# Performance work log

Measured on AMD Instinct MI355X. Metric: run time of the kernel, lower is better.

Reference implementation:

```python
import jax, jax.numpy as jnp
import numpy as np

MAX_WAVELENGTH = 10000.0
NUM_HEADS = 15
NUM_KV_HEADS = 5
HEAD_DIM = 64


def apply_rope(x, positions):
    """RoPE: x [B, L, H, D], positions [B, L] (int)."""
    d_half = x.shape[-1] // 2
    x = x.astype(jnp.float32)
    freq_exponents = (2.0 / x.shape[-1]) * jnp.arange(d_half, dtype=jnp.float32)
    timescale = MAX_WAVELENGTH ** freq_exponents  # [d_half]
    radians = positions[..., None].astype(jnp.float32) / timescale  # [B, L, d_half]
    radians = radians[..., None, :]  # [B, L, 1, d_half]
    sin, cos = jnp.sin(radians), jnp.cos(radians)
    x1, x2 = x[..., :d_half], x[..., d_half:]
    return jnp.concatenate([x1 * cos - x2 * sin, x2 * cos + x1 * sin], axis=-1)


def setup_inputs() -> dict:
    key = jax.random.key(0)
    k1, k2, k3, k4 = jax.random.split(key, 4)
    B, L = 2, 2048
    query_states = jax.random.normal(k1, (B, L, NUM_HEADS, HEAD_DIM), dtype=jnp.float32)
    key_states = jax.random.normal(k2, (B, L, NUM_KV_HEADS, HEAD_DIM), dtype=jnp.float32)
    value_states = jax.random.normal(k3, (B, L, NUM_KV_HEADS, HEAD_DIM), dtype=jnp.float32)
    positions = jnp.sort(jax.random.randint(k4, (B, L), 0, L, dtype=jnp.int32), axis=-1)
    # Causal (prefix-LM) boolean mask [B, L, L]
    attention_mask = jnp.broadcast_to(jnp.tril(jnp.ones((L, L), dtype=bool)), (B, L, L))
    return {
        "query_states": query_states,
        "key_states": key_states,
        "value_states": value_states,
        "positions": positions,
        "attention_mask": attention_mask,
    }


def reference(query_states, key_states, value_states, positions, attention_mask):
    B, L = query_states.shape[0], query_states.shape[1]
    groups = NUM_HEADS // NUM_KV_HEADS  # 3

    # RoPE on Q and K (eager, per original module)
    q = apply_rope(query_states, positions)  # [B, L, 15, 64] fp32
    k = apply_rope(key_states, positions)    # [B, L, 5, 64]  fp32

    # GQA expansion: [B, L, Kv, D] -> [B, L, Kv*groups, D]
    k = jnp.repeat(k, groups, axis=2)
    v = jnp.repeat(value_states, groups, axis=2).astype(jnp.float32)

    # Scores in fp32: [B, H, Lq, Lk]
    scores = jnp.einsum("bqhd,bkhd->bhqk", q, k) * (HEAD_DIM ** -0.5)
    big_neg = jnp.finfo(jnp.float32).min
    scores = jnp.where(attention_mask[:, None, :, :], scores, big_neg)
    probs = jax.nn.softmax(scores, axis=-1)

    out = jnp.einsum("bhqk,bkhd->bqhd", probs, v)  # [B, L, H, D]
    return out.reshape(B, L, NUM_HEADS * HEAD_DIM)  # [B, L, 960]
```

## Files before the change

kernel.cpp:

```cpp
#include <hip/hip_runtime.h>
#include <math.h>

#define NB 2
#define NL 2048
#define NHQ 15
#define NKV 5
#define HD 64
#define NT 32
#define GRP 3
#define PST 72
#define NG 16
#define SLOTF 2080

typedef __attribute__((ext_vector_type(8))) short short8;
typedef __attribute__((ext_vector_type(4))) float floatx4;

#define ROPE_C 0.28782313662425575f
#define QSCALE 0.18033688011116016f

__device__ __forceinline__ ushort f2bf(float x) {
    unsigned u = __builtin_bit_cast(unsigned, x);
    u = (u + 0x7FFFu + ((u >> 16) & 1u)) >> 16;
    return (ushort)u;
}
__device__ __forceinline__ unsigned pk2(float a, float b) {
    unsigned ua = __builtin_bit_cast(unsigned, a) + 0x8000u;
    unsigned ub = __builtin_bit_cast(unsigned, b) + 0x8000u;
    return __builtin_amdgcn_perm(ub, ua, 0x07060302u);
}
__device__ __forceinline__ void async16(ushort* lds, const ushort* g) {
    __builtin_amdgcn_global_load_lds(
        (const __attribute__((address_space(1))) unsigned int*)g,
        (__attribute__((address_space(3))) unsigned int*)lds, 16, 0, 0);
}

union U8  { short8 v; ushort u[8]; };
union F8  { float4 f4[2]; float f[8]; };

__global__ __launch_bounds__(256)
void prep_kv(const float* __restrict__ K, const float* __restrict__ V,
             const int* __restrict__ pos, ushort* __restrict__ Kr,
             ushort* __restrict__ Vr) {
    __shared__ float Vs[64][65];
    const int bid = blockIdx.x, t = threadIdx.x;
    if (bid < NB * NKV * NT) {
        int b = bid / (NKV * NT), rem = bid % (NKV * NT);
        int h = rem / NT, k0 = (rem % NT) * 64;
        int j = t >> 2, c0 = t & 3;
        int row = k0 + j;
        const float* src = K + ((size_t)((b * NL + row) * NKV + h)) * HD;
        int db = c0 * 8;
        F8 x1, x2;
        x1.f4[0] = *(const float4*)&src[db];
        x1.f4[1] = *(const float4*)&src[db + 4];
        x2.f4[0] = *(const float4*)&src[db + 32];
        x2.f4[1] = *(const float4*)&src[db + 36];
        float ps = (float)pos[b * NL + row];
        U8 lo, hi;
#pragma unroll
        for (int i = 0; i < 8; ++i) {
            float inv = __expf((float)(db + i) * -ROPE_C);
            float sn, cs; __sincosf(ps * inv, &sn, &cs);
            lo.u[i] = f2bf(x1.f[i] * cs - x2.f[i] * sn);
            hi.u[i] = f2bf(x2.f[i] * cs + x1.f[i] * sn);
        }
        ushort* dst = Kr + (size_t)bid * 4096;
        *(short8*)&dst[(j * 8 + (c0 ^ (j & 7))) * 8]       = lo.v;
        *(short8*)&dst[(j * 8 + ((c0 + 4) ^ (j & 7))) * 8] = hi.v;
    } else {
        int vb = bid - NB * NKV * NT;
        int b = vb / (NKV * NT), rem = vb % (NKV * NT);
        int h = rem / NT, k0 = (rem % NT) * 64;
#pragma unroll
        for (int it = 0; it < 4; ++it) {
            int e = t + it * 256;
            int j = e >> 4, d4 = (e & 15) * 4;
            *(float4*)&Vs[j][d4] =
                *(const float4*)&V[((size_t)((b * NL + k0 + j) * NKV + h)) * HD + d4];
        }
        __syncthreads();
        ushort* dst = Vr + (size_t)vb * 4096;
#pragma unroll
        for (int it = 0; it < 2; ++it) {
            int o = t + it * 256;
            int d = o >> 3, c = o & 7, j0 = c * 8;
            U8 r;
#pragma unroll
            for (int k = 0; k < 8; ++k) r.u[k] = f2bf(Vs[j0 + k][d]);
            *(short8*)&dst[(d * 8 + (c ^ (d & 7))) * 8] = r.v;
        }
    }
}

__global__ __launch_bounds__(256, 4)
void attn_partial(const float* __restrict__ Q, const ushort* __restrict__ Kr,
                  const ushort* __restrict__ Vr, const int* __restrict__ pos,
                  float* __restrict__ Pw, int CH, int TOT) {
    __shared__ __align__(16) ushort Kb[4096];
    __shared__ __align__(16) ushort Vb[4096];
    __shared__ __align__(16) ushort Pb[4][2][16 * PST];

    const int t = threadIdx.x;
    const int w = t >> 6, lane = t & 63;
    const int l16 = lane & 15, quad = lane >> 4;
    const int h = blockIdx.y, b = blockIdx.z;
    const int kvh = h / GRP;
    const int fidx = TOT - 1 - (int)blockIdx.x;

    int g = 0, chunk = fidx;
    for (; g < NG; ++g) {
        int nc = (2 * g + 2 + CH - 1) / CH;
        if (chunk < nc) break;
        chunk -= nc;
    }
    const int ntg = 2 * g + 2;
    const int kb0 = chunk * CH;
    int kb1 = kb0 + CH; if (kb1 > ntg) kb1 = ntg;
    const int qi = 4 * g + w;
    const int ntw = (qi >> 1) + 1;
    const int r0 = qi * 32;

    short8 Qa[2][2];
#pragma unroll
    for (int rf = 0; rf < 2; ++rf) {
        int row = r0 + rf * 16 + l16;
        const float* src = Q + ((size_t)((b * NL + row) * NHQ + h)) * HD;
        int db = quad * 8;
        F8 x1, x2;
        x1.f4[0] = *(const float4*)&src[db];
        x1.f4[1] = *(const float4*)&src[db + 4];
        x2.f4[0] = *(const float4*)&src[db + 32];
        x2.f4[1] = *(const float4*)&src[db + 36];
        float ps = (float)pos[b * NL + row];
        union { short8 v; unsigned u[4]; } lo, hi;
#pragma unroll
        for (int i = 0; i < 8; i += 2) {
            float inv0 = __expf((float)(db + i) * -ROPE_C);
            float inv1 = __expf((float)(db + i + 1) * -ROPE_C);
            float sn0, cs0, sn1, cs1;
            __sincosf(ps * inv0, &sn0, &cs0);
            __sincosf(ps * inv1, &sn1, &cs1);
            float l0 = (x1.f[i] * cs0 - x2.f[i] * sn0) * QSCALE;
            float l1 = (x1.f[i + 1] * cs1 - x2.f[i + 1] * sn1) * QSCALE;
            float h0 = (x2.f[i] * cs0 + x1.f[i] * sn0) * QSCALE;
            float h1 = (x2.f[i + 1] * cs1 + x1.f[i + 1] * sn1) * QSCALE;
            lo.u[i >> 1] = pk2(l0, l1);
            hi.u[i >> 1] = pk2(h0, h1);
        }
        Qa[rf][0] = lo.v;
        Qa[rf][1] = hi.v;
    }

    floatx4 O[2][4];
    float lsum[2] = {0.f, 0.f};
#pragma unroll
    for (int rf = 0; rf < 2; ++rf)
#pragma unroll
        for (int d = 0; d < 4; ++d) O[rf][d] = (floatx4){0.f, 0.f, 0.f, 0.f};

    const ushort* Kt0 = Kr + (size_t)((b * NKV + kvh) * NT) * 4096;
    const ushort* Vt0 = Vr + (size_t)((b * NKV + kvh) * NT) * 4096;
    const int swz8[2] = { ((quad)     ^ (l16 & 7)) * 8,
                          ((quad + 4) ^ (l16 & 7)) * 8 };

    for (int kb = kb0; kb < kb1; ++kb) {
        {
            const ushort* Kt = Kt0 + (size_t)kb * 4096;
            const ushort* Vt = Vt0 + (size_t)kb * 4096;
            int so = w * 1024;
#pragma unroll
            for (int i2 = 0; i2 < 2; ++i2) {
                int uo = so + i2 * 512;
                async16(&Kb[uo], Kt + uo + lane * 8);
                async16(&Vb[uo], Vt + uo + lane * 8);
            }
        }
        __syncthreads();

        if (kb < ntw) {
            floatx4 S[2][4];
#pragma unroll
            for (int rf = 0; rf < 2; ++rf)
#pragma unroll
                for (int c = 0; c < 4; ++c) S[rf][c] = (floatx4){0.f, 0.f, 0.f, 0.f};
#pragma unroll
            for (int s = 0; s < 2; ++s)
#pragma unroll
                for (int c = 0; c < 4; ++c) {
                    short8 kfv = *(const short8*)&Kb[(c * 16 + l16) * 64 + swz8[s]];
                    S[0][c] = __builtin_amdgcn_mfma_f32_16x16x32_bf16(kfv, Qa[0][s], S[0][c], 0, 0, 0);
                    S[1][c] = __builtin_amdgcn_mfma_f32_16x16x32_bf16(kfv, Qa[1][s], S[1][c], 0, 0, 0);
                }

            const bool diag = (kb == ntw - 1);
#pragma unroll
            for (int rf = 0; rf < 2; ++rf) {
                int qrow = r0 + rf * 16 + l16;
                float acc = 0.f;
#pragma unroll
                for (int c = 0; c < 4; ++c) {
                    float p[4];
#pragma unroll
                    for (int r = 0; r < 4; ++r) {
                        int key = kb * 64 + c * 16 + quad * 4 + r;
                        float sv = S[rf][c][r];
                        if (diag && key > qrow) sv = -1e30f;
                        p[r] = exp2f(sv);
                        acc += p[r];
                    }
                    *(uint2*)&Pb[w][rf][l16 * PST + c * 16 + quad * 4] =
                        make_uint2(pk2(p[0], p[1]), pk2(p[2], p[3]));
                }
                lsum[rf] += acc;
            }

#pragma unroll
            for (int s = 0; s < 2; ++s) {
                short8 pf0 = *(const short8*)&Pb[w][0][l16 * PST + s * 32 + quad * 8];
                short8 pf1 = *(const short8*)&Pb[w][1][l16 * PST + s * 32 + quad * 8];
#pragma unroll
                for (int d = 0; d < 4; ++d) {
                    short8 vfv = *(const short8*)&Vb[(d * 16 + l16) * 64 + swz8[s]];
                    O[0][d] = __builtin_amdgcn_mfma_f32_16x16x32_bf16(vfv, pf0, O[0][d], 0, 0, 0);
                    O[1][d] = __builtin_amdgcn_mfma_f32_16x16x32_bf16(vfv, pf1, O[1][d], 0, 0, 0);
                }
            }
        }
        __syncthreads();
    }

    float* slot = Pw + (((size_t)(b * NHQ + h) * TOT + fidx) * 4 + w) * SLOTF;
#pragma unroll
    for (int rf = 0; rf < 2; ++rf) {
#pragma unroll
        for (int d = 0; d < 4; ++d) {
            float4 o = make_float4(O[rf][d][0], O[rf][d][1], O[rf][d][2], O[rf][d][3]);
            *(float4*)&slot[(rf * 16 + l16) * 64 + d * 16 + quad * 4] = o;
        }
        float ls = lsum[rf];
        ls += __shfl_xor(ls, 16, 64);
        ls += __shfl_xor(ls, 32, 64);
        if (quad == 0) slot[2048 + rf * 16 + l16] = ls;
    }
}

__global__ __launch_bounds__(256)
void combine(const float* __restrict__ Pw, float* __restrict__ out,
             int CH, int TOT) {
    __shared__ float ls[32];
    const int qi = blockIdx.x;
    const int bh = blockIdx.y;
    const int b = bh / NHQ, h = bh % NHQ;
    const int g = qi >> 2, w = qi & 3;
    const int nch = (2 * g + 2 + CH - 1) / CH;
    int pfx = 0;
    for (int gg = 0; gg < g; ++gg) pfx += (2 * gg + 2 + CH - 1) / CH;
    const float* base = Pw + (((size_t)bh * TOT + pfx) * 4 + w) * SLOTF;

    const int t = threadIdx.x;
    const int rl = t >> 3, d0 = (t & 7) * 8;
    float a[8];
#pragma unroll
    for (int k = 0; k < 8; ++k) a[k] = 0.f;
    float lacc = 0.f;
    for (int c = 0; c < nch; ++c) {
        const float* pb = base + (size_t)c * 4 * SLOTF;
        float4 x0 = *(const float4*)&pb[rl * 64 + d0];
        float4 x1 = *(const float4*)&pb[rl * 64 + d0 + 4];
        a[0] += x0.x; a[1] += x0.y; a[2] += x0.z; a[3] += x0.w;
        a[4] += x1.x; a[5] += x1.y; a[6] += x1.z; a[7] += x1.w;
        if (t < 32) lacc += pb[2048 + t];
    }
    if (t < 32) ls[t] = lacc;
    __syncthreads();
    float rinv = 1.0f / ls[rl];
    float* op = out + (size_t)(b * NL + qi * 32 + rl) * (NHQ * HD) + h * HD + d0;
    *(float4*)&op[0] = make_float4(a[0] * rinv, a[1] * rinv, a[2] * rinv, a[3] * rinv);
    *(float4*)&op[4] = make_float4(a[4] * rinv, a[5] * rinv, a[6] * rinv, a[7] * rinv);
}

extern "C" void kernel_launch(void* const* d_in, const int* in_sizes, int n_in,
                              void* d_out, int out_size, void* d_ws, size_t ws_size,
                              hipStream_t stream) {
    const float* Q   = (const float*)d_in[0];
    const float* K   = (const float*)d_in[1];
    const float* V   = (const float*)d_in[2];
    const int*   pos = (const int*)d_in[3];
    ushort* Kr = (ushort*)d_ws;
    ushort* Vr = Kr + (size_t)NB * NKV * NT * 4096;
    float*  Pw = (float*)(Vr + (size_t)NB * NKV * NT * 4096);
    float*  out = (float*)d_out;
    const size_t prepBytes = (size_t)2 * NB * NKV * NT * 4096 * sizeof(ushort);

    int CH = 32, TOT = NG;
    const int ladder[3] = {4, 8, 16};
    for (int i = 0; i < 3; ++i) {
        int ch = ladder[i], tot = 0;
        for (int gq = 0; gq < NG; ++gq) tot += (2 * gq + 2 + ch - 1) / ch;
        size_t need = prepBytes + (size_t)NB * NHQ * tot * 4 * SLOTF * sizeof(float);
        if (need <= ws_size) { CH = ch; TOT = tot; break; }
    }
    if (CH == 32) { TOT = NG; }

    prep_kv<<<2 * NB * NKV * NT, 256, 0, stream>>>(K, V, pos, Kr, Vr);
    dim3 grid(TOT, NHQ, NB);
    attn_partial<<<grid, 256, 0, stream>>>(Q, Kr, Vr, pos, Pw, CH, TOT);
    combine<<<dim3(NL / 32, NB * NHQ), 256, 0, stream>>>(Pw, out, CH, TOT);
}
```

Baseline: 160.6 us.

## Double-buffer K/V tiles and write single-chunk query groups directly to output

Adds ping-pong LDS buffers for K and V so the next tile's async load is issued before computing on the current one, hiding global load latency. Query groups whose key range fits in a single chunk now normalize and write the final output directly, and the combine kernel is launched only for the remaining groups. The split-size ladder drops the 4-tile option, giving fewer, larger chunks. This doubles K/V LDS use, which may lower occupancy, and coarser chunks reduce parallelism for long rows.

Measured after the change: 154.2 us. 1.04x faster.

```diff
diff --git a/kernel.cpp b/kernel.cpp
--- a/kernel.cpp
+++ b/kernel.cpp
@@ -95,9 +95,10 @@
 __global__ __launch_bounds__(256, 4)
 void attn_partial(const float* __restrict__ Q, const ushort* __restrict__ Kr,
                   const ushort* __restrict__ Vr, const int* __restrict__ pos,
-                  float* __restrict__ Pw, int CH, int TOT) {
-    __shared__ __align__(16) ushort Kb[4096];
-    __shared__ __align__(16) ushort Vb[4096];
+                  float* __restrict__ Pw, float* __restrict__ out,
+                  int CH, int TOT) {
+    __shared__ __align__(16) ushort Kb[2][4096];
+    __shared__ __align__(16) ushort Vb[2][4096];
     __shared__ __align__(16) ushort Pb[4][2][16 * PST];
 
     const int t = threadIdx.x;
@@ -114,6 +115,7 @@
         chunk -= nc;
     }
     const int ntg = 2 * g + 2;
+    const int nc  = (ntg + CH - 1) / CH;
     const int kb0 = chunk * CH;
     int kb1 = kb0 + CH; if (kb1 > ntg) kb1 = ntg;
     const int qi = 4 * g + w;
@@ -162,20 +164,28 @@
     const ushort* Vt0 = Vr + (size_t)((b * NKV + kvh) * NT) * 4096;
     const int swz8[2] = { ((quad)     ^ (l16 & 7)) * 8,
                           ((quad + 4) ^ (l16 & 7)) * 8 };
-
-    for (int kb = kb0; kb < kb1; ++kb) {
-        {
-            const ushort* Kt = Kt0 + (size_t)kb * 4096;
-            const ushort* Vt = Vt0 + (size_t)kb * 4096;
-            int so = w * 1024;
-#pragma unroll
-            for (int i2 = 0; i2 < 2; ++i2) {
-                int uo = so + i2 * 512;
-                async16(&Kb[uo], Kt + uo + lane * 8);
-                async16(&Vb[uo], Vt + uo + lane * 8);
-            }
-        }
-        __syncthreads();
+    const int so = w * 1024;
+
+    {
+        const ushort* Kt = Kt0 + (size_t)kb0 * 4096;
+        const ushort* Vt = Vt0 + (size_t)kb0 * 4096;
+        async16(&Kb[0][so],       Kt + so + lane * 8);
+        async16(&Kb[0][so + 512], Kt + so + 512 + lane * 8);
+        async16(&Vb[0][so],       Vt + so + lane * 8);
+        async16(&Vb[0][so + 512], Vt + so + 512 + lane * 8);
+    }
+    __syncthreads();
+
+    int p = 0;
+    for (int kb = kb0; kb < kb1; ++kb, p ^= 1) {
+        if (kb + 1 < kb1) {
+            const ushort* Kt = Kt0 + (size_t)(kb + 1) * 4096;
+            const ushort* Vt = Vt0 + (size_t)(kb + 1) * 4096;
+            async16(&Kb[p ^ 1][so],       Kt + so + lane * 8);
+            async16(&Kb[p ^ 1][so + 512], Kt + so + 512 + lane * 8);
+            async16(&Vb[p ^ 1][so],       Vt + so + lane * 8);
+            async16(&Vb[p ^ 1][so + 512], Vt + so + 512 + lane * 8);
+        }
 
         if (kb < ntw) {
             floatx4 S[2][4];
@@ -187,7 +197,7 @@
             for (int s = 0; s < 2; ++s)
 #pragma unroll
                 for (int c = 0; c < 4; ++c) {
-                    short8 kfv = *(const short8*)&Kb[(c * 16 + l16) * 64 + swz8[s]];
+                    short8 kfv = *(const short8*)&Kb[p][(c * 16 + l16) * 64 + swz8[s]];
                     S[0][c] = __builtin_amdgcn_mfma_f32_16x16x32_bf16(kfv, Qa[0][s], S[0][c], 0, 0, 0);
                     S[1][c] = __builtin_amdgcn_mfma_f32_16x16x32_bf16(kfv, Qa[1][s], S[1][c], 0, 0, 0);
                 }
@@ -199,17 +209,17 @@
                 float acc = 0.f;
 #pragma unroll
                 for (int c = 0; c < 4; ++c) {
-                    float p[4];
+                    float pv[4];
 #pragma unroll
                     for (int r = 0; r < 4; ++r) {
                         int key = kb * 64 + c * 16 + quad * 4 + r;
                         float sv = S[rf][c][r];
                         if (diag && key > qrow) sv = -1e30f;
-                        p[r] = exp2f(sv);
-                        acc += p[r];
+                        pv[r] = exp2f(sv);
+                        acc += pv[r];
                     }
                     *(uint2*)&Pb[w][rf][l16 * PST + c * 16 + quad * 4] =
-                        make_uint2(pk2(p[0], p[1]), pk2(p[2], p[3]));
+                        make_uint2(pk2(pv[0], pv[1]), pk2(pv[2], pv[3]));
                 }
                 lsum[rf] += acc;
             }
@@ -220,7 +230,7 @@
                 short8 pf1 = *(const short8*)&Pb[w][1][l16 * PST + s * 32 + quad * 8];
 #pragma unroll
                 for (int d = 0; d < 4; ++d) {
-                    short8 vfv = *(const short8*)&Vb[(d * 16 + l16) * 64 + swz8[s]];
+                    short8 vfv = *(const short8*)&Vb[p][(d * 16 + l16) * 64 + swz8[s]];
                     O[0][d] = __builtin_amdgcn_mfma_f32_16x16x32_bf16(vfv, pf0, O[0][d], 0, 0, 0);
                     O[1][d] = __builtin_amdgcn_mfma_f32_16x16x32_bf16(vfv, pf1, O[1][d], 0, 0, 0);
                 }
@@ -229,26 +239,44 @@
         __syncthreads();
     }
 
-    float* slot = Pw + (((size_t)(b * NHQ + h) * TOT + fidx) * 4 + w) * SLOTF;
-#pragma unroll
-    for (int rf = 0; rf < 2; ++rf) {
-#pragma unroll
-        for (int d = 0; d < 4; ++d) {
-            float4 o = make_float4(O[rf][d][0], O[rf][d][1], O[rf][d][2], O[rf][d][3]);
-            *(float4*)&slot[(rf * 16 + l16) * 64 + d * 16 + quad * 4] = o;
-        }
-        float ls = lsum[rf];
-        ls += __shfl_xor(ls, 16, 64);
-        ls += __shfl_xor(ls, 32, 64);
-        if (quad == 0) slot[2048 + rf * 16 + l16] = ls;
+    if (nc == 1) {
+#pragma unroll
+        for (int rf = 0; rf < 2; ++rf) {
+            float ls = lsum[rf];
+            ls += __shfl_xor(ls, 16, 64);
+            ls += __shfl_xor(ls, 32, 64);
+            float rinv = 1.0f / ls;
+            int qrow = r0 + rf * 16 + l16;
+            float* op = out + (size_t)(b * NL + qrow) * (NHQ * HD) + h * HD;
+#pragma unroll
+            for (int d = 0; d < 4; ++d) {
+                float4 o = make_float4(O[rf][d][0] * rinv, O[rf][d][1] * rinv,
+                                       O[rf][d][2] * rinv, O[rf][d][3] * rinv);
+                *(float4*)&op[d * 16 + quad * 4] = o;
+            }
+        }
+    } else {
+        float* slot = Pw + (((size_t)(b * NHQ + h) * TOT + fidx) * 4 + w) * SLOTF;
+#pragma unroll
+        for (int rf = 0; rf < 2; ++rf) {
+#pragma unroll
+            for (int d = 0; d < 4; ++d) {
+                float4 o = make_float4(O[rf][d][0], O[rf][d][1], O[rf][d][2], O[rf][d][3]);
+                *(float4*)&slot[(rf * 16 + l16) * 64 + d * 16 + quad * 4] = o;
+            }
+            float ls = lsum[rf];
+            ls += __shfl_xor(ls, 16, 64);
+            ls += __shfl_xor(ls, 32, 64);
+            if (quad == 0) slot[2048 + rf * 16 + l16] = ls;
+        }
     }
 }
 
 __global__ __launch_bounds__(256)
 void combine(const float* __restrict__ Pw, float* __restrict__ out,
-             int CH, int TOT) {
+             int CH, int TOT, int qi0) {
     __shared__ float ls[32];
-    const int qi = blockIdx.x;
+    const int qi = qi0 + blockIdx.x;
     const int bh = blockIdx.y;
     const int b = bh / NHQ, h = bh % NHQ;
     const int g = qi >> 2, w = qi & 3;
@@ -293,17 +321,18 @@
     const size_t prepBytes = (size_t)2 * NB * NKV * NT * 4096 * sizeof(ushort);
 
     int CH = 32, TOT = NG;
-    const int ladder[3] = {4, 8, 16};
-    for (int i = 0; i < 3; ++i) {
+    const int ladder[2] = {8, 16};
+    for (int i = 0; i < 2; ++i) {
         int ch = ladder[i], tot = 0;
         for (int gq = 0; gq < NG; ++gq) tot += (2 * gq + 2 + ch - 1) / ch;
         size_t need = prepBytes + (size_t)NB * NHQ * tot * 4 * SLOTF * sizeof(float);
         if (need <= ws_size) { CH = ch; TOT = tot; break; }
     }
-    if (CH == 32) { TOT = NG; }
 
     prep_kv<<<2 * NB * NKV * NT, 256, 0, stream>>>(K, V, pos, Kr, Vr);
     dim3 grid(TOT, NHQ, NB);
-    attn_partial<<<grid, 256, 0, stream>>>(Q, Kr, Vr, pos, Pw, CH, TOT);
-    combine<<<dim3(NL / 32, NB * NHQ), 256, 0, stream>>>(Pw, out, CH, TOT);
-}
+    attn_partial<<<grid, 256, 0, stream>>>(Q, Kr, Vr, pos, Pw, out, CH, TOT);
+    int qi0 = 2 * CH;
+    if (qi0 < 64)
+        combine<<<dim3(64 - qi0, NB * NHQ), 256, 0, stream>>>(Pw, out, CH, TOT, qi0);
+}
```
